# Optimization experiments

Hardware: AMD Instinct MI355X
Metric: run time of the kernel (lower is better)

The kernel has to match this reference:

```python
import jax, jax.numpy as jnp
import numpy as np

N_NODES, N_EDGES = 16000, 256000
M_IN_S, M_IN_V = 16, 8   # input irreps: 16x0e + 8x1o (dim 40)
M_K_S, M_K_V = 8, 4      # key/query irreps: 8x0e + 4x1o
M_V_S, M_V_V = 16, 8     # value irreps: 16x0e + 8x1o
NUM_BASIS, R_CUT = 32, 2.5
SQ3 = 1.7320508075688772  # sqrt(3)


def _fc_net(r, W1, W2):
    # e3nn FullyConnectedNet([num_basis,16,numels], silu): weight-normalized linears
    h = jax.nn.silu(r @ (W1 / jnp.sqrt(jnp.float32(W1.shape[0]))))
    return h @ (W2 / jnp.sqrt(jnp.float32(W2.shape[0])))


def _edge_tp(xs, xv, y0, y1, w, m1s, m1v, mos, mov):
    # FullyConnectedTensorProduct(in1 = m1s x0e + m1v x1o, in2 = 1x0e + 1x1o,
    #   out = mos x0e + mov x1o), per-edge external weights w [E, numels].
    # Paths: 0e*0e->0e, 1o*1o->0e (dot/sqrt3), 0e*1o->1o, 1o*0e->1o.
    E = w.shape[0]
    n1, n2, n3 = m1s * mos, m1v * mos, m1s * mov
    w_ss = w[:, :n1].reshape(E, m1s, mos)
    w_vv = w[:, n1:n1 + n2].reshape(E, m1v, mos)
    w_sv = w[:, n1 + n2:n1 + n2 + n3].reshape(E, m1s, mov)
    w_vs = w[:, n1 + n2 + n3:].reshape(E, m1v, mov)
    inv = 1.0 / jnp.sqrt(jnp.float32(m1s + m1v))  # fan-in path normalization
    out_s = (jnp.einsum('ei,eio->eo', xs * y0[:, None], w_ss)
             + jnp.einsum('eic,ec,eio->eo', xv, y1, w_vv) / SQ3) * inv
    out_v = (jnp.einsum('ei,ec,eio->eoc', xs, y1, w_sv)
             + jnp.einsum('eic,eio->eoc', xv * y0[:, None, None], w_vs)) * inv
    return out_s, out_v


def _forward(pos, x, Wq_s, Wq_v, Wk1, Wk2, Wv1, Wv2, Ws_ss, Ws_vv, edge_src, edge_dst):
    xs, xv = x[:, :M_IN_S], x[:, M_IN_S:].reshape(-1, M_IN_V, 3)
    vec = pos[edge_dst] - pos[edge_src]                       # [E,3]
    d = jnp.linalg.norm(vec, axis=1)
    d_safe = jnp.maximum(d, 1e-6)
    # bessel radial basis with cutoff (soft_one_hot_linspace, basis='bessel') * sqrt(num_basis)
    n = jnp.arange(1, NUM_BASIS + 1, dtype=jnp.float32)
    rad = jnp.sqrt(2.0 / R_CUT) * jnp.sin(n[None] * jnp.pi * d_safe[:, None] / R_CUT) / d_safe[:, None]
    rad = jnp.where((d < R_CUT)[:, None], rad, 0.0) * jnp.sqrt(jnp.float32(NUM_BASIS))
    # spherical harmonics lmax=1, normalize=True, component normalization
    vh = vec / d_safe[:, None]
    y0, y1 = jnp.ones_like(d), SQ3 * vh
    # query projection (o3.Linear: per-irrep linear with 1/sqrt(fan_in))
    q_s = xs @ Wq_s / jnp.sqrt(jnp.float32(M_IN_S))           # [N, M_K_S]
    q_v = jnp.einsum('nic,io->noc', xv, Wq_v) / jnp.sqrt(jnp.float32(M_IN_V))
    # per-edge tensor-product weights from radial MLPs (shared_weights=False)
    wk = _fc_net(rad, Wk1, Wk2)                               # [E, 288]
    wv = _fc_net(rad, Wv1, Wv2)                               # [E, 576]
    xs_e, xv_e = xs[edge_src], xv[edge_src]
    k_s, k_v = _edge_tp(xs_e, xv_e, y0, y1, wk, M_IN_S, M_IN_V, M_K_S, M_K_V)
    v_s, v_v = _edge_tp(xs_e, xv_e, y0, y1, wv, M_IN_S, M_IN_V, M_V_S, M_V_V)
    # similarity tensor product (query x key -> 0e), shared internal weights
    fan = jnp.sqrt(jnp.float32(M_K_S * M_K_S + M_K_V * M_K_V))
    sim = (jnp.einsum('ei,ij,ej->e', q_s[edge_dst], Ws_ss, k_s)
           + jnp.einsum('eic,ij,ejc->e', q_v[edge_dst], Ws_vv, k_v) / SQ3) / fan
    # scatter softmax over incoming edges of each dst node
    attn = jnp.exp(sim)
    Z = jax.ops.segment_sum(attn, edge_dst, num_segments=N_NODES)
    a = attn / Z[edge_dst]
    # weighted scatter-sum aggregation
    out_s = jax.ops.segment_sum(a[:, None] * v_s, edge_dst, num_segments=N_NODES)
    out_v = jax.ops.segment_sum(a[:, None, None] * v_v, edge_dst, num_segments=N_NODES)
    return jnp.concatenate([out_s, out_v.reshape(N_NODES, -1)], axis=1)  # [N, 40]


def setup_inputs() -> dict:
    key = jax.random.key(0)
    ks = jax.random.split(key, 12)
    wk_numels = M_IN_S * M_K_S + M_IN_V * M_K_S + M_IN_S * M_K_V + M_IN_V * M_K_V  # 288
    wv_numels = M_IN_S * M_V_S + M_IN_V * M_V_S + M_IN_S * M_V_V + M_IN_V * M_V_V  # 576
    return {
        'pos': jax.random.uniform(ks[0], (N_NODES, 3), jnp.float32) * 3.0,
        'x': jax.random.normal(ks[1], (N_NODES, M_IN_S + 3 * M_IN_V), jnp.float32),
        'Wq_s': jax.random.normal(ks[2], (M_IN_S, M_K_S), jnp.float32),
        'Wq_v': jax.random.normal(ks[3], (M_IN_V, M_K_V), jnp.float32),
        'Wk1': jax.random.normal(ks[4], (NUM_BASIS, 16), jnp.float32),
        'Wk2': jax.random.normal(ks[5], (16, wk_numels), jnp.float32),
        'Wv1': jax.random.normal(ks[6], (NUM_BASIS, 16), jnp.float32),
        'Wv2': jax.random.normal(ks[7], (16, wv_numels), jnp.float32),
        'Ws_ss': jax.random.normal(ks[8], (M_K_S, M_K_S), jnp.float32) * 0.1,
        'Ws_vv': jax.random.normal(ks[9], (M_K_V, M_K_V), jnp.float32) * 0.1,
        'edge_src': jax.random.randint(ks[10], (N_EDGES,), 0, N_NODES),
        'edge_dst': jax.random.randint(ks[11], (N_EDGES,), 0, N_NODES),
    }


def reference(pos, x, Wq_s, Wq_v, Wk1, Wk2, Wv1, Wv2, Ws_ss, Ws_vv, edge_src, edge_dst):
    return _forward(pos, x, Wq_s, Wq_v, Wk1, Wk2, Wv1, Wv2, Ws_ss, Ws_vv, edge_src, edge_dst)
```

## Files before the change

### kernel.cpp

```cpp
#include <hip/hip_runtime.h>
#include <hip/hip_bf16.h>

#define N_NODES 16000
#define N_EDGES 256000

#define OFF_SD     0
#define OFF_SIMB   512000
#define OFF_CNT    768000
#define OFF_START  784000
#define OFF_CUR    800001
#define OFF_WB     816004
#define OFF_WBK    834436
#define OFF_QT     846724
#define OFF_Z      1006724

typedef _Float16 f16x2 __attribute__((ext_vector_type(2)));
typedef _Float16 f16x8v __attribute__((ext_vector_type(8)));
typedef float f32x4v __attribute__((ext_vector_type(4)));

__device__ __forceinline__ float fdot2f(f16x2 a, f16x2 b, float c) {
#if __has_builtin(__builtin_amdgcn_fdot2)
  return __builtin_amdgcn_fdot2(a, b, c, false);
#else
  return fmaf((float)a.x, (float)b.x, fmaf((float)a.y, (float)b.y, c));
#endif
}

__device__ __forceinline__ unsigned packh2(float a, float b) {
  union { unsigned u; f16x2 p; } v;
  v.p.x = (_Float16)a; v.p.y = (_Float16)b;
  return v.u;
}

__device__ __forceinline__ unsigned splat_half(unsigned x, unsigned sel) {
#if __has_builtin(__builtin_amdgcn_perm)
  return __builtin_amdgcn_perm(x, x, sel);
#else
  unsigned h = (sel == 0x03020302u) ? (x >> 16) : (x & 0xffffu);
  return h | (h << 16);
#endif
}

__device__ __forceinline__ void load_row40(const float* __restrict__ p, float* xr) {
  const float4* rp = reinterpret_cast<const float4*>(p);
#pragma unroll
  for (int q = 0; q < 10; ++q) {
    float4 f = rp[q];
    xr[4 * q + 0] = f.x; xr[4 * q + 1] = f.y; xr[4 * q + 2] = f.z; xr[4 * q + 3] = f.w;
  }
}

struct EdgeGeom { float vhx, vhy, vhz, y1x, y1y, y1z; };

__device__ __forceinline__ void edge_h_pk(const float* __restrict__ pos, int s, int d,
                                          const unsigned* W1, f16x2* hp, EdgeGeom& g) {
  float vx = pos[3 * d + 0] - pos[3 * s + 0];
  float vy = pos[3 * d + 1] - pos[3 * s + 1];
  float vz = pos[3 * d + 2] - pos[3 * s + 2];
  float dist = sqrtf(fmaf(vx, vx, fmaf(vy, vy, vz * vz)));
  float dsafe = fmaxf(dist, 1e-6f);
  float rinv = 1.0f / dsafe;
  g.vhx = vx * rinv; g.vhy = vy * rinv; g.vhz = vz * rinv;
  g.y1x = 1.7320508075688772f * g.vhx;
  g.y1y = 1.7320508075688772f * g.vhy;
  g.y1z = 1.7320508075688772f * g.vhz;
  float pre[16];
#pragma unroll
  for (int t = 0; t < 16; ++t) pre[t] = 0.f;
  float sx, cx;
  sincosf(1.2566370614359172f * dsafe, &sx, &cx);
  cx = fminf(1.f, fmaxf(-1.f, cx));
  float twoc = 2.f * cx;
  float sprev = 0.f, scur = sx;
  float rscale = (dist < 2.5f) ? (5.059644256269407f * rinv) : 0.f;
#pragma unroll
  for (int bp = 0; bp < 16; ++bp) {
    float r0 = rscale * scur;
    float sn = fmaf(twoc, scur, -sprev); sprev = scur; scur = sn;
    float r1 = rscale * scur;
    sn = fmaf(twoc, scur, -sprev); sprev = scur; scur = sn;
    union { unsigned u; f16x2 p; } rp; rp.p.x = (_Float16)r0; rp.p.y = (_Float16)r1;
    union { uint4 u[4]; f16x2 p[16]; } w;
    w.u[0] = *(const uint4*)(W1 + bp * 16);
    w.u[1] = *(const uint4*)(W1 + bp * 16 + 4);
    w.u[2] = *(const uint4*)(W1 + bp * 16 + 8);
    w.u[3] = *(const uint4*)(W1 + bp * 16 + 12);
#pragma unroll
    for (int t = 0; t < 16; ++t) pre[t] = fdot2f(rp.p, w.p[t], pre[t]);
  }
#pragma unroll
  for (int tp = 0; tp < 8; ++tp) {
    float h0 = pre[2 * tp]     / (1.f + __expf(-pre[2 * tp]));
    float h1 = pre[2 * tp + 1] / (1.f + __expf(-pre[2 * tp + 1]));
    hp[tp].x = (_Float16)h0; hp[tp].y = (_Float16)h1;
  }
}

__global__ void k_hist(const int* __restrict__ edst, int* __restrict__ cnt) {
  int e = blockIdx.x * 256 + threadIdx.x;
  atomicAdd(&cnt[edst[e]], 1);
}

__global__ void __launch_bounds__(1024) k_scan(const int* __restrict__ cnt,
                                               int* __restrict__ start, int* __restrict__ cur) {
  __shared__ int part[1024];
  int t = threadIdx.x;
  int base = t * 16;
  int local[16];
  int sum = 0;
#pragma unroll
  for (int i = 0; i < 16; ++i) {
    int idx = base + i;
    int c = (idx < N_NODES) ? cnt[idx] : 0;
    local[i] = sum; sum += c;
  }
  part[t] = sum;
  __syncthreads();
  for (int off = 1; off < 1024; off <<= 1) {
    int v = (t >= off) ? part[t - off] : 0;
    __syncthreads();
    part[t] += v;
    __syncthreads();
  }
  int prev = (t == 0) ? 0 : part[t - 1];
#pragma unroll
  for (int i = 0; i < 16; ++i) {
    int idx = base + i;
    if (idx < N_NODES) { int st = prev + local[i]; start[idx] = st; cur[idx] = st; }
  }
  if (t == 0) start[N_NODES] = N_EDGES;
}

__global__ void k_fill(const int* __restrict__ esrc, const int* __restrict__ edst,
                       int* __restrict__ cur, int2* __restrict__ sd) {
  int e = blockIdx.x * 256 + threadIdx.x;
  int d = edst[e];
  int slot = atomicAdd(&cur[d], 1);
  sd[slot] = make_int2(esrc[e], d);
}

#define PREP_ZERO_B   2625
#define PREP_PB_B     144
#define PREP_PBK_B    96
#define PREP_NQ_B     63
#define PREP_TOTAL_B  (PREP_ZERO_B + PREP_PB_B + PREP_PBK_B + PREP_NQ_B)

__global__ void __launch_bounds__(256) k_prep(
    const float* __restrict__ x,
    const float* __restrict__ Wq_s, const float* __restrict__ Wq_v,
    const float* __restrict__ Wss, const float* __restrict__ Wvv,
    const float* __restrict__ Wk2, const float* __restrict__ Wv2,
    int* __restrict__ cnt, float* __restrict__ Z, float* __restrict__ out,
    unsigned short* __restrict__ WB, unsigned short* __restrict__ WBK,
    unsigned short* __restrict__ QT) {
  int b = blockIdx.x;
  if (b < PREP_ZERO_B) {
    int i = b * 256 + threadIdx.x;
    if (i < 16000)       cnt[i] = 0;
    else if (i < 32000)  Z[i - 16000] = 0.f;
    else                 out[i - 32000] = 0.f;
    return;
  }
  b -= PREP_ZERO_B;
  if (b < PREP_PB_B) {
    int idx = b * 256 + threadIdx.x;
    int j = idx & 7;
    int lane = (idx >> 3) & 63;
    int t3 = idx >> 9;
    int ct = t3 % 3, kk = t3 / 3;
    int q = lane >> 4, m = lane & 15;
    int row = 32 * kk + 8 * q + j;
    int col = 16 * ct + m;
    int t = row & 15;
    float v = 0.f;
    if (row < 256) {
      int i = row >> 4;
      if (col < 16)      v = Wv2[t * 576 + i * 16 + col];
      else if (col < 24) v = Wv2[t * 576 + 384 + i * 8 + (col - 16)];
    } else if (row < 384) {
      int i = (row - 256) >> 4;
      if (col < 16)      v = Wv2[t * 576 + 256 + i * 16 + col];
    } else {
      int part = (row - 384) >> 7;
      int i = ((row - 384) & 127) >> 4;
      int cb = 24 + 8 * part;
      if (col >= cb && col < cb + 8) v = Wv2[t * 576 + 512 + i * 8 + (col - cb)];
    }
    union { unsigned short u; _Float16 h; } cv;
    cv.h = (_Float16)(v * 0.051031036307982884f);
    WB[idx] = cv.u;
    return;
  }
  b -= PREP_PB_B;
  if (b < PREP_PBK_B) {
    int idx = b * 256 + threadIdx.x;
    int j = idx & 7;
    int lane = (idx >> 3) & 63;
    int t2 = idx >> 9;
    int ct = t2 & 1, kk = t2 >> 1;
    int q = lane >> 4, m = lane & 15;
    int row = 32 * kk + 8 * q + j;
    int col = 16 * ct + m;
    int t = row & 15;
    float v = 0.f;
    if (col < 24) {
      if (row < 256) {
        int i = row >> 4;
        if (col < 8)       v = Wk2[t * 288 + i * 8 + col];
        else if (col < 12) v = Wk2[t * 288 + 192 + i * 4 + (col - 8)];
      } else if (row < 384) {
        int i = (row - 256) >> 4;
        if (col < 8)       v = Wk2[t * 288 + 128 + i * 8 + col];
      } else {
        int c = (row - 384) >> 7;
        int i = ((row - 384) & 127) >> 4;
        int cb = 12 + 4 * c;
        if (col >= cb && col < cb + 4) v = Wk2[t * 288 + 256 + i * 4 + (col - cb)];
      }
    }
    union { unsigned short u; _Float16 h; } cv;
    cv.h = (_Float16)(v * 0.051031036307982884f);
    WBK[idx] = cv.u;
    return;
  }
  b -= PREP_PBK_B;
  __shared__ float Ls[240];
  if (threadIdx.x < 240) {
    int i = threadIdx.x;
    float v;
    if (i < 128)      v = Wq_s[i] * 0.25f;
    else if (i < 160) v = Wq_v[i - 128] * 0.3535533905932738f;
    else if (i < 224) v = Wss[i - 160] * 0.11180339887498948f;
    else              v = Wvv[i - 224] * 0.06454972243679028f;
    Ls[i] = v;
  }
  __syncthreads();
  int n = b * 256 + threadIdx.x;
  if (n >= N_NODES) return;
  float xd[40];
  load_row40(x + 40 * n, xd);
  float qd[8], qvd[12];
#pragma unroll
  for (int o = 0; o < 8; ++o) qd[o] = 0.f;
#pragma unroll
  for (int i = 0; i < 16; ++i)
#pragma unroll
    for (int o = 0; o < 8; ++o) qd[o] = fmaf(xd[i], Ls[8 * i + o], qd[o]);
#pragma unroll
  for (int k = 0; k < 12; ++k) qvd[k] = 0.f;
#pragma unroll
  for (int i = 0; i < 8; ++i)
#pragma unroll
    for (int o = 0; o < 4; ++o)
#pragma unroll
      for (int c = 0; c < 3; ++c)
        qvd[3 * o + c] = fmaf(xd[16 + 3 * i + c], Ls[128 + 4 * i + o], qvd[3 * o + c]);
  float qf[20];
#pragma unroll
  for (int j = 0; j < 8; ++j) {
    float t = 0.f;
#pragma unroll
    for (int i = 0; i < 8; ++i) t = fmaf(qd[i], Ls[160 + 8 * i + j], t);
    qf[j] = t;
  }
#pragma unroll
  for (int o = 0; o < 4; ++o)
#pragma unroll
    for (int c = 0; c < 3; ++c) {
      float t = 0.f;
#pragma unroll
      for (int i = 0; i < 4; ++i) t = fmaf(qvd[3 * i + c], Ls[224 + 4 * i + o], t);
      qf[8 + 3 * o + c] = t;
    }
  uint2* qp = (uint2*)(QT + 20 * n);
#pragma unroll
  for (int bq = 0; bq < 5; ++bq) {
    uint2 st;
    st.x = packh2(qf[4 * bq], qf[4 * bq + 1]);
    st.y = packh2(qf[4 * bq + 2], qf[4 * bq + 3]);
    qp[bq] = st;
  }
}

#define RSTR 36

__device__ __forceinline__ void build_coef(const float* xr, const float* Bv, float* coef) {
#pragma unroll
  for (int i = 0; i < 16; ++i) coef[i] = xr[i];
#pragma unroll
  for (int i = 0; i < 8; ++i) coef[16 + i] = Bv[i];
#pragma unroll
  for (int p = 0; p < 4; ++p)
#pragma unroll
    for (int c = 0; c < 3; ++c) {
      coef[24 + 8 * c + 2 * p]     = xr[16 + 6 * p + c];
      coef[24 + 8 * c + 2 * p + 1] = xr[16 + 6 * p + 3 + c];
    }
}

__global__ void __launch_bounds__(64) k_edge1(
    const float* __restrict__ pos, const float* __restrict__ x,
    const float* __restrict__ Wk1, const unsigned short* __restrict__ WBK,
    const unsigned short* __restrict__ QT,
    const int2* __restrict__ sd, float* __restrict__ simb, float* __restrict__ Z) {
  __shared__ __align__(16) unsigned LW1[256];
  __shared__ __align__(16) unsigned SM[64 * RSTR];

  for (int i = threadIdx.x; i < 256; i += 64) {
    int bp = i >> 4, t = i & 15;
    LW1[i] = packh2(Wk1[(2 * bp) * 16 + t] * 0.17677669529663687f,
                    Wk1[(2 * bp + 1) * 16 + t] * 0.17677669529663687f);
  }
  __syncthreads();

  int lane = threadIdx.x;
  int q = lane >> 4, m = lane & 15;
  int q1 = q & 1;
  unsigned seld = (q >> 1) ? 0x03020302u : 0x01000100u;
  int slot = blockIdx.x * 64 + threadIdx.x;
  int2 e = sd[slot];
  int s = e.x, d = e.y;

  f16x2 hp[8]; EdgeGeom g;
  edge_h_pk(pos, s, d, LW1, hp, g);

  float qf[20];
  {
    const uint2* qp = (const uint2*)(QT + 20 * d);
#pragma unroll
    for (int b = 0; b < 5; ++b) {
      uint2 u = qp[b];
      union { unsigned d; f16x2 p; } a0, a1;
      a0.d = u.x; a1.d = u.y;
      qf[4 * b] = (float)a0.p.x; qf[4 * b + 1] = (float)a0.p.y;
      qf[4 * b + 2] = (float)a1.p.x; qf[4 * b + 3] = (float)a1.p.y;
    }
  }

  float xr[40];
  load_row40(x + 40 * s, xr);
  float Bv[8];
#pragma unroll
  for (int i = 0; i < 8; ++i)
    Bv[i] = fmaf(xr[16 + 3 * i], g.vhx, fmaf(xr[17 + 3 * i], g.vhy, xr[18 + 3 * i] * g.vhz));
  float coef[48];
  build_coef(xr, Bv, coef);

  unsigned* row = &SM[lane * RSTR];
  {
    union { uint4 u; f16x2 p[4]; } h0, h1;
#pragma unroll
    for (int k = 0; k < 4; ++k) { h0.p[k] = hp[k]; h1.p[k] = hp[4 + k]; }
    *(uint4*)(row) = h0.u;
    *(uint4*)(row + 4) = h1.u;
  }
#pragma unroll
  for (int bt = 0; bt < 6; ++bt) {
    uint4 w;
    w.x = packh2(coef[8 * bt + 0], coef[8 * bt + 1]);
    w.y = packh2(coef[8 * bt + 2], coef[8 * bt + 3]);
    w.z = packh2(coef[8 * bt + 4], coef[8 * bt + 5]);
    w.w = packh2(coef[8 * bt + 6], coef[8 * bt + 7]);
    *(uint4*)(row + 8 + 4 * bt) = w;
  }
  unsigned* wbase = &SM[0];
  union { uint4 u; f16x2 p[4]; } hs[4];
#pragma unroll
  for (int rt = 0; rt < 4; ++rt)
    hs[rt].u = *(const uint4*)(wbase + (16 * rt + m) * RSTR + 4 * q1);

  const uint4* WBq = (const uint4*)WBK;
  f32x4v acc[4][2];
#pragma unroll
  for (int rt = 0; rt < 4; ++rt)
#pragma unroll
    for (int ct = 0; ct < 2; ++ct) { f32x4v z = {0.f, 0.f, 0.f, 0.f}; acc[rt][ct] = z; }

#pragma unroll
  for (int bt = 0; bt < 6; ++bt) {
    union { uint4 u; unsigned d[4]; } cb[4];
#pragma unroll
    for (int rt = 0; rt < 4; ++rt)
      cb[rt].u = *(const uint4*)(wbase + (16 * rt + m) * RSTR + 8 + 4 * bt);
#pragma unroll
    for (int t = 0; t < 4; ++t) {
      int kk = 4 * bt + t;
      union { uint4 u; f16x2 p[4]; f16x8v v; } av[4];
#pragma unroll
      for (int rt = 0; rt < 4; ++rt) {
        union { unsigned d; f16x2 p; } sp;
        sp.d = splat_half(cb[rt].d[t], seld);
#pragma unroll
        for (int w = 0; w < 4; ++w) av[rt].p[w] = hs[rt].p[w] * sp.p;
      }
#pragma unroll
      for (int ct = 0; ct < 2; ++ct) {
        union { uint4 u; f16x8v v; } bf;
        bf.u = WBq[(kk * 2 + ct) * 64 + lane];
#pragma unroll
        for (int rt = 0; rt < 4; ++rt)
          acc[rt][ct] = __builtin_amdgcn_mfma_f32_16x16x32_f16(av[rt].v, bf.v, acc[rt][ct], 0, 0, 0);
      }
    }
  }

  float P[24];
  float* ctb = (float*)wbase;
#pragma unroll
  for (int rt = 0; rt < 4; ++rt)
#pragma unroll
    for (int r = 0; r < 4; ++r)
      ctb[m * 65 + 16 * rt + 4 * q + r] = acc[rt][0][r];
#pragma unroll
  for (int o = 0; o < 16; ++o) P[o] = ctb[o * 65 + lane];
#pragma unroll
  for (int rt = 0; rt < 4; ++rt)
#pragma unroll
    for (int r = 0; r < 4; ++r)
      ctb[m * 65 + 16 * rt + 4 * q + r] = acc[rt][1][r];
#pragma unroll
  for (int o = 0; o < 8; ++o) P[16 + o] = ctb[o * 65 + lane];

  float sim = 0.f;
#pragma unroll
  for (int j = 0; j < 8; ++j) sim = fmaf(qf[j], P[j], sim);
  float y1c[3] = {g.y1x, g.y1y, g.y1z};
#pragma unroll
  for (int o = 0; o < 4; ++o)
#pragma unroll
    for (int c = 0; c < 3; ++c)
      sim = fmaf(qf[8 + 3 * o + c], fmaf(y1c[c], P[8 + o], P[12 + 4 * c + o]), sim);

  float ev = __expf(sim);
  simb[slot] = ev;
  bool same[6];
#pragma unroll
  for (int k = 0; k < 6; ++k) {
    int dd = __shfl_down(d, 1 << k, 64);
    same[k] = ((lane + (1 << k)) < 64) && (dd == d);
  }
  int dprev = __shfl_up(d, 1, 64);
  bool head = (lane == 0) || (dprev != d);
  float v = ev;
#pragma unroll
  for (int k = 0; k < 6; ++k) {
    float ov = __shfl_down(v, 1 << k, 64);
    v += same[k] ? ov : 0.f;
  }
  if (head) atomicAdd(&Z[d], v);
}

__global__ void __launch_bounds__(64) k_edge2(
    const float* __restrict__ pos, const float* __restrict__ x,
    const float* __restrict__ Wv1, const unsigned short* __restrict__ WB,
    const int2* __restrict__ sd, const float* __restrict__ eb,
    const float* __restrict__ Zv, float* __restrict__ out) {
  __shared__ __align__(16) unsigned LW1[256];
  __shared__ __align__(16) unsigned SM[64 * RSTR];

  for (int i = threadIdx.x; i < 256; i += 64) {
    int bp = i >> 4, t = i & 15;
    LW1[i] = packh2(Wv1[(2 * bp) * 16 + t] * 0.17677669529663687f,
                    Wv1[(2 * bp + 1) * 16 + t] * 0.17677669529663687f);
  }
  __syncthreads();

  int lane = threadIdx.x;
  int q = lane >> 4, m = lane & 15;
  int q1 = q & 1;
  unsigned seld = (q >> 1) ? 0x03020302u : 0x01000100u;
  int slot = blockIdx.x * 64 + threadIdx.x;
  int2 e = sd[slot];
  int s = e.x, d = e.y;

  float ev = eb[slot];
  float Zd = Zv[d];

  bool same[6];
#pragma unroll
  for (int k = 0; k < 6; ++k) {
    int dd = __shfl_down(d, 1 << k, 64);
    same[k] = ((lane + (1 << k)) < 64) && (dd == d);
  }
  int dprev = __shfl_up(d, 1, 64);
  bool head = (lane == 0) || (dprev != d);

  f16x2 hp[8]; EdgeGeom g;
  edge_h_pk(pos, s, d, LW1, hp, g);
  float xr[40];
  load_row40(x + 40 * s, xr);
  float Bv[8];
#pragma unroll
  for (int i = 0; i < 8; ++i)
    Bv[i] = fmaf(xr[16 + 3 * i], g.vhx, fmaf(xr[17 + 3 * i], g.vhy, xr[18 + 3 * i] * g.vhz));
  float coef[48];
  build_coef(xr, Bv, coef);
  float a = ev / Zd;

  unsigned* row = &SM[lane * RSTR];
  {
    union { uint4 u; f16x2 p[4]; } h0, h1;
#pragma unroll
    for (int k = 0; k < 4; ++k) { h0.p[k] = hp[k]; h1.p[k] = hp[4 + k]; }
    *(uint4*)(row) = h0.u;
    *(uint4*)(row + 4) = h1.u;
  }
#pragma unroll
  for (int bt = 0; bt < 6; ++bt) {
    uint4 w;
    w.x = packh2(coef[8 * bt + 0], coef[8 * bt + 1]);
    w.y = packh2(coef[8 * bt + 2], coef[8 * bt + 3]);
    w.z = packh2(coef[8 * bt + 4], coef[8 * bt + 5]);
    w.w = packh2(coef[8 * bt + 6], coef[8 * bt + 7]);
    *(uint4*)(row + 8 + 4 * bt) = w;
  }
  unsigned* wbase = &SM[0];
  union { uint4 u; f16x2 p[4]; } hs[4];
#pragma unroll
  for (int rt = 0; rt < 4; ++rt)
    hs[rt].u = *(const uint4*)(wbase + (16 * rt + m) * RSTR + 4 * q1);

  const uint4* WBq = (const uint4*)WB;
  f32x4v acc[4][3];
#pragma unroll
  for (int rt = 0; rt < 4; ++rt)
#pragma unroll
    for (int ct = 0; ct < 3; ++ct) { f32x4v z = {0.f, 0.f, 0.f, 0.f}; acc[rt][ct] = z; }

#pragma unroll
  for (int bt = 0; bt < 6; ++bt) {
    union { uint4 u; unsigned d[4]; } cb[4];
#pragma unroll
    for (int rt = 0; rt < 4; ++rt)
      cb[rt].u = *(const uint4*)(wbase + (16 * rt + m) * RSTR + 8 + 4 * bt);
#pragma unroll
    for (int t = 0; t < 4; ++t) {
      int kk = 4 * bt + t;
      union { uint4 u; f16x2 p[4]; f16x8v v; } av[4];
#pragma unroll
      for (int rt = 0; rt < 4; ++rt) {
        union { unsigned d; f16x2 p; } sp;
        sp.d = splat_half(cb[rt].d[t], seld);
#pragma unroll
        for (int w = 0; w < 4; ++w) av[rt].p[w] = hs[rt].p[w] * sp.p;
      }
#pragma unroll
      for (int ct = 0; ct < 3; ++ct) {
        union { uint4 u; f16x8v v; } bf;
        bf.u = WBq[(kk * 3 + ct) * 64 + lane];
#pragma unroll
        for (int rt = 0; rt < 4; ++rt)
          acc[rt][ct] = __builtin_amdgcn_mfma_f32_16x16x32_f16(av[rt].v, bf.v, acc[rt][ct], 0, 0, 0);
      }
    }
  }

  float* ctb = (float*)wbase;
  float* op = out + 40 * d;

  {
#pragma unroll
    for (int rt = 0; rt < 4; ++rt)
#pragma unroll
      for (int r = 0; r < 4; ++r)
        ctb[m * 65 + 16 * rt + 4 * q + r] = acc[rt][0][r];
    float P0[16];
#pragma unroll
    for (int o = 0; o < 16; ++o) P0[o] = ctb[o * 65 + lane];
#pragma unroll
    for (int o = 0; o < 16; ++o) {
      float v = a * P0[o];
#pragma unroll
      for (int k = 0; k < 6; ++k) {
        float ov = __shfl_down(v, 1 << k, 64);
        v += same[k] ? ov : 0.f;
      }
      if (head) atomicAdd(op + o, v);
    }
  }
  float P1[16], P2[16];
#pragma unroll
  for (int rt = 0; rt < 4; ++rt)
#pragma unroll
    for (int r = 0; r < 4; ++r)
      ctb[m * 65 + 16 * rt + 4 * q + r] = acc[rt][1][r];
#pragma unroll
  for (int o = 0; o < 16; ++o) P1[o] = ctb[o * 65 + lane];
#pragma unroll
  for (int rt = 0; rt < 4; ++rt)
#pragma unroll
    for (int r = 0; r < 4; ++r)
      ctb[m * 65 + 16 * rt + 4 * q + r] = acc[rt][2][r];
#pragma unroll
  for (int o = 0; o < 16; ++o) P2[o] = ctb[o * 65 + lane];
#pragma unroll
  for (int o = 0; o < 8; ++o) {
    float s1v = P1[o];
    float vc[3];
    vc[0] = a * fmaf(g.y1x, s1v, P1[8 + o]);
    vc[1] = a * fmaf(g.y1y, s1v, P2[o]);
    vc[2] = a * fmaf(g.y1z, s1v, P2[8 + o]);
#pragma unroll
    for (int c = 0; c < 3; ++c) {
      float v = vc[c];
#pragma unroll
      for (int k = 0; k < 6; ++k) {
        float ov = __shfl_down(v, 1 << k, 64);
        v += same[k] ? ov : 0.f;
      }
      if (head) atomicAdd(op + 16 + 3 * o + c, v);
    }
  }
}

extern "C" void kernel_launch(void* const* d_in, const int* in_sizes, int n_in,
                              void* d_out, int out_size, void* d_ws, size_t ws_size,
                              hipStream_t stream) {
  (void)in_sizes; (void)n_in; (void)out_size; (void)ws_size;
  const float* pos  = (const float*)d_in[0];
  const float* x    = (const float*)d_in[1];
  const float* Wq_s = (const float*)d_in[2];
  const float* Wq_v = (const float*)d_in[3];
  const float* Wk1  = (const float*)d_in[4];
  const float* Wk2  = (const float*)d_in[5];
  const float* Wv1  = (const float*)d_in[6];
  const float* Wv2  = (const float*)d_in[7];
  const float* Wss  = (const float*)d_in[8];
  const float* Wvv  = (const float*)d_in[9];
  const int* esrc = (const int*)d_in[10];
  const int* edst = (const int*)d_in[11];
  int*   wsi  = (int*)d_ws;
  float* wsf  = (float*)d_ws;
  float* out  = (float*)d_out;

  int2*  sd    = (int2*)(wsi + OFF_SD);
  float* simb  = wsf + OFF_SIMB;
  int*   cnt   = wsi + OFF_CNT;
  int*   start = wsi + OFF_START;
  int*   cur   = wsi + OFF_CUR;
  unsigned short* WB  = (unsigned short*)(wsf + OFF_WB);
  unsigned short* WBK = (unsigned short*)(wsf + OFF_WBK);
  unsigned short* QT  = (unsigned short*)(wsf + OFF_QT);
  float* Z    = wsf + OFF_Z;

  k_prep<<<PREP_TOTAL_B, 256, 0, stream>>>(x, Wq_s, Wq_v, Wss, Wvv, Wk2, Wv2,
                                           cnt, Z, out, WB, WBK, QT);
  k_hist<<<1000, 256, 0, stream>>>(edst, cnt);
  k_scan<<<1, 1024, 0, stream>>>(cnt, start, cur);
  k_fill<<<1000, 256, 0, stream>>>(esrc, edst, cur, sd);
  k_edge1<<<4000, 64, 0, stream>>>(pos, x, Wk1, WBK, QT, sd, simb, Z);
  k_edge2<<<4000, 64, 0, stream>>>(pos, x, Wv1, WB, sd, simb, Z, out);
}
```

Before: 220.2 us.

## Stage MFMA weight tiles in LDS across waves and replace block scan with atomics

The edge kernels now run four waves per block. Each block cooperatively streams the per-k-step B weight tiles into double-buffered LDS with global_load_lds, so one copy is shared by all four waves instead of every wave fetching the tiles from global memory. The single-block prefix scan is replaced by a per-node atomicAdd on a global counter. That still gives each destination a contiguous segment, but the segments are no longer in node order. The trade-offs are extra block-wide barriers on every k-step, higher LDS use that may cut occupancy, and one more zero-init in the prep kernel.

```diff
diff --git a/kernel.cpp b/kernel.cpp
--- a/kernel.cpp
+++ b/kernel.cpp
@@ -13,6 +13,7 @@
 #define OFF_WBK    834436
 #define OFF_QT     846724
 #define OFF_Z      1006724
+#define OFF_GT     1022724
 
 typedef _Float16 f16x2 __attribute__((ext_vector_type(2)));
 typedef _Float16 f16x8v __attribute__((ext_vector_type(8)));
@@ -38,6 +39,15 @@
 #else
   unsigned h = (sel == 0x03020302u) ? (x >> 16) : (x & 0xffffu);
   return h | (h << 16);
+#endif
+}
+
+__device__ __forceinline__ void gload_lds16(const unsigned* g, unsigned* l) {
+#if __has_builtin(__builtin_amdgcn_global_load_lds)
+  __builtin_amdgcn_global_load_lds((const __attribute__((address_space(1))) unsigned*)g,
+                                   (__attribute__((address_space(3))) unsigned*)l, 16, 0, 0);
+#else
+  *(uint4*)l = *(const uint4*)g;
 #endif
 }
 
@@ -101,34 +111,10 @@
   atomicAdd(&cnt[edst[e]], 1);
 }
 
-__global__ void __launch_bounds__(1024) k_scan(const int* __restrict__ cnt,
-                                               int* __restrict__ start, int* __restrict__ cur) {
-  __shared__ int part[1024];
-  int t = threadIdx.x;
-  int base = t * 16;
-  int local[16];
-  int sum = 0;
-#pragma unroll
-  for (int i = 0; i < 16; ++i) {
-    int idx = base + i;
-    int c = (idx < N_NODES) ? cnt[idx] : 0;
-    local[i] = sum; sum += c;
-  }
-  part[t] = sum;
-  __syncthreads();
-  for (int off = 1; off < 1024; off <<= 1) {
-    int v = (t >= off) ? part[t - off] : 0;
-    __syncthreads();
-    part[t] += v;
-    __syncthreads();
-  }
-  int prev = (t == 0) ? 0 : part[t - 1];
-#pragma unroll
-  for (int i = 0; i < 16; ++i) {
-    int idx = base + i;
-    if (idx < N_NODES) { int st = prev + local[i]; start[idx] = st; cur[idx] = st; }
-  }
-  if (t == 0) start[N_NODES] = N_EDGES;
+__global__ void k_scan2(const int* __restrict__ cnt, int* __restrict__ cur,
+                        int* __restrict__ gtot) {
+  int n = blockIdx.x * 256 + threadIdx.x;
+  if (n < N_NODES) cur[n] = atomicAdd(gtot, cnt[n]);
 }
 
 __global__ void k_fill(const int* __restrict__ esrc, const int* __restrict__ edst,
@@ -139,7 +125,7 @@
   sd[slot] = make_int2(esrc[e], d);
 }
 
-#define PREP_ZERO_B   2625
+#define PREP_ZERO_B   2626
 #define PREP_PB_B     144
 #define PREP_PBK_B    96
 #define PREP_NQ_B     63
@@ -152,13 +138,14 @@
     const float* __restrict__ Wk2, const float* __restrict__ Wv2,
     int* __restrict__ cnt, float* __restrict__ Z, float* __restrict__ out,
     unsigned short* __restrict__ WB, unsigned short* __restrict__ WBK,
-    unsigned short* __restrict__ QT) {
+    unsigned short* __restrict__ QT, int* __restrict__ gtot) {
   int b = blockIdx.x;
   if (b < PREP_ZERO_B) {
     int i = b * 256 + threadIdx.x;
     if (i < 16000)       cnt[i] = 0;
     else if (i < 32000)  Z[i - 16000] = 0.f;
-    else                 out[i - 32000] = 0.f;
+    else if (i < 672000) out[i - 32000] = 0.f;
+    else if (i == 672000) *gtot = 0;
     return;
   }
   b -= PREP_ZERO_B;
@@ -298,26 +285,28 @@
     }
 }
 
-__global__ void __launch_bounds__(64) k_edge1(
+__global__ void __launch_bounds__(256) k_edge1(
     const float* __restrict__ pos, const float* __restrict__ x,
     const float* __restrict__ Wk1, const unsigned short* __restrict__ WBK,
     const unsigned short* __restrict__ QT,
     const int2* __restrict__ sd, float* __restrict__ simb, float* __restrict__ Z) {
   __shared__ __align__(16) unsigned LW1[256];
-  __shared__ __align__(16) unsigned SM[64 * RSTR];
-
-  for (int i = threadIdx.x; i < 256; i += 64) {
+  __shared__ __align__(16) unsigned SM[4][64 * RSTR];
+  __shared__ __align__(16) unsigned BB[2][2048];
+
+  {
+    int i = threadIdx.x;
     int bp = i >> 4, t = i & 15;
     LW1[i] = packh2(Wk1[(2 * bp) * 16 + t] * 0.17677669529663687f,
                     Wk1[(2 * bp + 1) * 16 + t] * 0.17677669529663687f);
   }
   __syncthreads();
 
-  int lane = threadIdx.x;
+  int wave = threadIdx.x >> 6, lane = threadIdx.x & 63;
   int q = lane >> 4, m = lane & 15;
   int q1 = q & 1;
   unsigned seld = (q >> 1) ? 0x03020302u : 0x01000100u;
-  int slot = blockIdx.x * 64 + threadIdx.x;
+  int slot = blockIdx.x * 256 + threadIdx.x;
   int2 e = sd[slot];
   int s = e.x, d = e.y;
 
@@ -346,7 +335,7 @@
   float coef[48];
   build_coef(xr, Bv, coef);
 
-  unsigned* row = &SM[lane * RSTR];
+  unsigned* row = &SM[wave][lane * RSTR];
   {
     union { uint4 u; f16x2 p[4]; } h0, h1;
 #pragma unroll
@@ -363,7 +352,7 @@
     w.w = packh2(coef[8 * bt + 6], coef[8 * bt + 7]);
     *(uint4*)(row + 8 + 4 * bt) = w;
   }
-  unsigned* wbase = &SM[0];
+  unsigned* wbase = &SM[wave][0];
   union { uint4 u; f16x2 p[4]; } hs[4];
 #pragma unroll
   for (int rt = 0; rt < 4; ++rt)
@@ -377,14 +366,26 @@
     for (int ct = 0; ct < 2; ++ct) { f32x4v z = {0.f, 0.f, 0.f, 0.f}; acc[rt][ct] = z; }
 
 #pragma unroll
+  for (int j = 0; j < 2; ++j)
+    gload_lds16((const unsigned*)(WBq + j * 256 + threadIdx.x),
+                &BB[0][(j * 256 + threadIdx.x) * 4]);
+  __syncthreads();
+
+#pragma unroll
   for (int bt = 0; bt < 6; ++bt) {
+    if (bt < 5) {
+#pragma unroll
+      for (int j = 0; j < 2; ++j)
+        gload_lds16((const unsigned*)(WBq + (bt + 1) * 512 + j * 256 + threadIdx.x),
+                    &BB[(bt + 1) & 1][(j * 256 + threadIdx.x) * 4]);
+    }
     union { uint4 u; unsigned d[4]; } cb[4];
 #pragma unroll
     for (int rt = 0; rt < 4; ++rt)
       cb[rt].u = *(const uint4*)(wbase + (16 * rt + m) * RSTR + 8 + 4 * bt);
+    const uint4* Bq = (const uint4*)BB[bt & 1];
 #pragma unroll
     for (int t = 0; t < 4; ++t) {
-      int kk = 4 * bt + t;
       union { uint4 u; f16x2 p[4]; f16x8v v; } av[4];
 #pragma unroll
       for (int rt = 0; rt < 4; ++rt) {
@@ -396,12 +397,13 @@
 #pragma unroll
       for (int ct = 0; ct < 2; ++ct) {
         union { uint4 u; f16x8v v; } bf;
-        bf.u = WBq[(kk * 2 + ct) * 64 + lane];
+        bf.u = Bq[(t * 2 + ct) * 64 + lane];
 #pragma unroll
         for (int rt = 0; rt < 4; ++rt)
           acc[rt][ct] = __builtin_amdgcn_mfma_f32_16x16x32_f16(av[rt].v, bf.v, acc[rt][ct], 0, 0, 0);
       }
     }
+    __syncthreads();
   }
 
   float P[24];
@@ -450,26 +452,28 @@
   if (head) atomicAdd(&Z[d], v);
 }
 
-__global__ void __launch_bounds__(64) k_edge2(
+__global__ void __launch_bounds__(256) k_edge2(
     const float* __restrict__ pos, const float* __restrict__ x,
     const float* __restrict__ Wv1, const unsigned short* __restrict__ WB,
     const int2* __restrict__ sd, const float* __restrict__ eb,
     const float* __restrict__ Zv, float* __restrict__ out) {
   __shared__ __align__(16) unsigned LW1[256];
-  __shared__ __align__(16) unsigned SM[64 * RSTR];
-
-  for (int i = threadIdx.x; i < 256; i += 64) {
+  __shared__ __align__(16) unsigned SM[4][64 * RSTR];
+  __shared__ __align__(16) unsigned BB[2][3072];
+
+  {
+    int i = threadIdx.x;
     int bp = i >> 4, t = i & 15;
     LW1[i] = packh2(Wv1[(2 * bp) * 16 + t] * 0.17677669529663687f,
                     Wv1[(2 * bp + 1) * 16 + t] * 0.17677669529663687f);
   }
   __syncthreads();
 
-  int lane = threadIdx.x;
+  int wave = threadIdx.x >> 6, lane = threadIdx.x & 63;
   int q = lane >> 4, m = lane & 15;
   int q1 = q & 1;
   unsigned seld = (q >> 1) ? 0x03020302u : 0x01000100u;
-  int slot = blockIdx.x * 64 + threadIdx.x;
+  int slot = blockIdx.x * 256 + threadIdx.x;
   int2 e = sd[slot];
   int s = e.x, d = e.y;
 
@@ -497,7 +501,7 @@
   build_coef(xr, Bv, coef);
   float a = ev / Zd;
 
-  unsigned* row = &SM[lane * RSTR];
+  unsigned* row = &SM[wave][lane * RSTR];
   {
     union { uint4 u; f16x2 p[4]; } h0, h1;
 #pragma unroll
@@ -514,7 +518,7 @@
     w.w = packh2(coef[8 * bt + 6], coef[8 * bt + 7]);
     *(uint4*)(row + 8 + 4 * bt) = w;
   }
-  unsigned* wbase = &SM[0];
+  unsigned* wbase = &SM[wave][0];
   union { uint4 u; f16x2 p[4]; } hs[4];
 #pragma unroll
   for (int rt = 0; rt < 4; ++rt)
@@ -528,14 +532,26 @@
     for (int ct = 0; ct < 3; ++ct) { f32x4v z = {0.f, 0.f, 0.f, 0.f}; acc[rt][ct] = z; }
 
 #pragma unroll
+  for (int j = 0; j < 3; ++j)
+    gload_lds16((const unsigned*)(WBq + j * 256 + threadIdx.x),
+                &BB[0][(j * 256 + threadIdx.x) * 4]);
+  __syncthreads();
+
+#pragma unroll
   for (int bt = 0; bt < 6; ++bt) {
+    if (bt < 5) {
+#pragma unroll
+      for (int j = 0; j < 3; ++j)
+        gload_lds16((const unsigned*)(WBq + (bt + 1) * 768 + j * 256 + threadIdx.x),
+                    &BB[(bt + 1) & 1][(j * 256 + threadIdx.x) * 4]);
+    }
     union { uint4 u; unsigned d[4]; } cb[4];
 #pragma unroll
     for (int rt = 0; rt < 4; ++rt)
       cb[rt].u = *(const uint4*)(wbase + (16 * rt + m) * RSTR + 8 + 4 * bt);
+    const uint4* Bq = (const uint4*)BB[bt & 1];
 #pragma unroll
     for (int t = 0; t < 4; ++t) {
-      int kk = 4 * bt + t;
       union { uint4 u; f16x2 p[4]; f16x8v v; } av[4];
 #pragma unroll
       for (int rt = 0; rt < 4; ++rt) {
@@ -547,12 +563,13 @@
 #pragma unroll
       for (int ct = 0; ct < 3; ++ct) {
         union { uint4 u; f16x8v v; } bf;
-        bf.u = WBq[(kk * 3 + ct) * 64 + lane];
+        bf.u = Bq[(t * 3 + ct) * 64 + lane];
 #pragma unroll
         for (int rt = 0; rt < 4; ++rt)
           acc[rt][ct] = __builtin_amdgcn_mfma_f32_16x16x32_f16(av[rt].v, bf.v, acc[rt][ct], 0, 0, 0);
       }
     }
+    __syncthreads();
   }
 
   float* ctb = (float*)wbase;
@@ -636,18 +653,18 @@
   int2*  sd    = (int2*)(wsi + OFF_SD);
   float* simb  = wsf + OFF_SIMB;
   int*   cnt   = wsi + OFF_CNT;
-  int*   start = wsi + OFF_START;
   int*   cur   = wsi + OFF_CUR;
   unsigned short* WB  = (unsigned short*)(wsf + OFF_WB);
   unsigned short* WBK = (unsigned short*)(wsf + OFF_WBK);
   unsigned short* QT  = (unsigned short*)(wsf + OFF_QT);
   float* Z    = wsf + OFF_Z;
+  int*   gtot = wsi + OFF_GT;
 
   k_prep<<<PREP_TOTAL_B, 256, 0, stream>>>(x, Wq_s, Wq_v, Wss, Wvv, Wk2, Wv2,
-                                           cnt, Z, out, WB, WBK, QT);
+                                           cnt, Z, out, WB, WBK, QT, gtot);
   k_hist<<<1000, 256, 0, stream>>>(edst, cnt);
-  k_scan<<<1, 1024, 0, stream>>>(cnt, start, cur);
+  k_scan2<<<63, 256, 0, stream>>>(cnt, cur, gtot);
   k_fill<<<1000, 256, 0, stream>>>(esrc, edst, cur, sd);
-  k_edge1<<<4000, 64, 0, stream>>>(pos, x, Wk1, WBK, QT, sd, simb, Z);
-  k_edge2<<<4000, 64, 0, stream>>>(pos, x, Wv1, WB, sd, simb, Z, out);
-}
+  k_edge1<<<1000, 256, 0, stream>>>(pos, x, Wk1, WBK, QT, sd, simb, Z);
+  k_edge2<<<1000, 256, 0, stream>>>(pos, x, Wv1, WB, sd, simb, Z, out);
+}
```

Result: faster. 201.9 us (-8.3%).
